# Kernel tuning notes

Hardware: AMD Instinct MI355X
Metric: run time of the kernel (lower is better)

The kernel has to match this reference:

```python
import jax, jax.numpy as jnp
import numpy as np

NUM_HEADS = 16
D_MODEL = 1024
D_K = D_MODEL // NUM_HEADS


def setup_inputs() -> dict:
    key = jax.random.key(0)
    ks = jax.random.split(key, 11)
    B, S, D = 4, 2048, D_MODEL
    s = 1.0 / np.sqrt(D)
    return {
        "query": jax.random.normal(ks[0], (B, S, D), jnp.float32),
        "key": jax.random.normal(ks[1], (B, S, D), jnp.float32),
        "value": jax.random.normal(ks[2], (B, S, D), jnp.float32),
        "Wq": jax.random.normal(ks[3], (D, D), jnp.float32) * s,
        "bq": jnp.zeros((D,), jnp.float32),
        "Wk": jax.random.normal(ks[4], (D, D), jnp.float32) * s,
        "bk": jnp.zeros((D,), jnp.float32),
        "Wv": jax.random.normal(ks[5], (D, D), jnp.float32) * s,
        "bv": jnp.zeros((D,), jnp.float32),
        "Wo": jax.random.normal(ks[6], (D, D), jnp.float32) * s,
        "bo": jnp.zeros((D,), jnp.float32),
    }


def reference(query, key, value, Wq, bq, Wk, bk, Wv, bv, Wo, bo):
    B, S, D = query.shape
    H, dk = NUM_HEADS, D_K
    # linear projections (torch Linear: x @ W.T + b)
    q = query @ Wq.T + bq
    k = key @ Wk.T + bk
    v = value @ Wv.T + bv
    # [B, S, D] -> [B, H, S, dk]
    q = q.reshape(B, S, H, dk).transpose(0, 2, 1, 3)
    k = k.reshape(B, S, H, dk).transpose(0, 2, 1, 3)
    v = v.reshape(B, S, H, dk).transpose(0, 2, 1, 3)
    # scaled dot-product attention (explicit scores, no mask, dropout unused in fwd)
    scores = jnp.einsum("bhqd,bhkd->bhqk", q, k) / jnp.sqrt(jnp.float32(dk))
    attn = jax.nn.softmax(scores, axis=-1)
    out = jnp.einsum("bhqk,bhkd->bhqd", attn, v)
    out = out.transpose(0, 2, 1, 3).reshape(B, S, D)
    return out @ Wo.T + bo
```

## Files before the change

kernel.cpp:

```cpp
#include <hip/hip_runtime.h>
#include <cstdint>
#include <cstddef>

typedef __bf16 bf16_t;
typedef __bf16 bf16x8 __attribute__((ext_vector_type(8)));
typedef __bf16 bf16x4 __attribute__((ext_vector_type(4)));
typedef float f32x4 __attribute__((ext_vector_type(4)));

static constexpr int SEQ = 2048;
static constexpr int DMODEL = 1024;
static constexpr int HEADS = 16;
static constexpr int DK = 64;
static constexpr int MROWS = 4 * SEQ;
static constexpr size_t NEC = (size_t)MROWS * DMODEL;
static constexpr size_t WEC = (size_t)DMODEL * DMODEL;

__global__ __launch_bounds__(256) void cast_w(const float* __restrict__ wq,
                                              const float* __restrict__ wk,
                                              const float* __restrict__ wv,
                                              const float* __restrict__ wo,
                                              bf16_t* __restrict__ out) {
  size_t i = (size_t)blockIdx.x * 256 + threadIdx.x;
  size_t e = i * 8;
  const float* src;
  size_t off;
  if (e < WEC) { src = wq; off = e; }
  else if (e < 2 * WEC) { src = wk; off = e - WEC; }
  else if (e < 3 * WEC) { src = wv; off = e - 2 * WEC; }
  else { src = wo; off = e - 3 * WEC; }
  const float4* p = reinterpret_cast<const float4*>(src + off);
  float4 a = p[0], b = p[1];
  bf16x8 o;
  o[0] = (bf16_t)a.x; o[1] = (bf16_t)a.y; o[2] = (bf16_t)a.z; o[3] = (bf16_t)a.w;
  o[4] = (bf16_t)b.x; o[5] = (bf16_t)b.y; o[6] = (bf16_t)b.z; o[7] = (bf16_t)b.w;
  *(reinterpret_cast<bf16x8*>(out + e)) = o;
}

__device__ __forceinline__ void async16(const bf16_t* g, bf16_t* l) {
  __builtin_amdgcn_global_load_lds((const __attribute__((address_space(1))) void*)g,
                                   (__attribute__((address_space(3))) void*)l,
                                   16, 0, 0);
}

__device__ __forceinline__ int lds_off(int m, int l4) {
  int lr = m >> 1;
  return lr * 64 + (((((m & 1) << 2) | l4) ^ (lr & 7)) << 3);
}

__global__ __launch_bounds__(512, 4) void gemm_qkv(const float* __restrict__ Aq,
                                                   const float* __restrict__ Ak,
                                                   const float* __restrict__ Av,
                                                   const bf16_t* __restrict__ Wbase,
                                                   const float* __restrict__ bq,
                                                   const float* __restrict__ bk,
                                                   const float* __restrict__ bv,
                                                   float scaleQ,
                                                   bf16_t* __restrict__ QKbase,
                                                   bf16_t* __restrict__ Vt) {
  __shared__ __align__(16) bf16_t smem[24576];
  bf16_t* sAb = smem;
  bf16_t* sBb = smem + 8192;
  const int tid = threadIdx.x;
  const int lane = tid & 63;
  const int w = tid >> 6;
  const int wm = w >> 2, wn = w & 3;
  const int l16 = lane & 15, l4 = lane >> 4;

  int bid = blockIdx.x;
  int swz = (bid & 7) * 96 + (bid >> 3);
  const int seg = swz >> 8;
  const int inner = swz & 255;
  const float* Afp = seg == 0 ? Aq : (seg == 1 ? Ak : Av);
  const bf16_t* Bw = Wbase + (size_t)seg * WEC;
  const float* bias = seg == 0 ? bq : (seg == 1 ? bk : bv);
  const float scale = seg == 0 ? scaleQ : 1.0f;
  const int bm = inner >> 2, bn = inner & 3;
  const int m0 = bm << 7, n0 = bn << 8;

  const int sg = (lane & 7) ^ ((lane >> 3) & 7);
  const int mS = 2 * (w * 8 + (lane >> 3)) + (sg >> 2);
  const int gS = (sg & 3) * 8;

  f32x4 acc[4][4] = {};
  float4 ra0, ra1;

  auto loadA = [&](int k0) {
    const float* p = Afp + (size_t)(m0 + mS) * DMODEL + k0 + gS;
    ra0 = *reinterpret_cast<const float4*>(p);
    ra1 = *reinterpret_cast<const float4*>(p + 4);
  };
  auto writeA = [&](int bb) {
    bf16x8 o;
    o[0] = (bf16_t)ra0.x; o[1] = (bf16_t)ra0.y; o[2] = (bf16_t)ra0.z; o[3] = (bf16_t)ra0.w;
    o[4] = (bf16_t)ra1.x; o[5] = (bf16_t)ra1.y; o[6] = (bf16_t)ra1.z; o[7] = (bf16_t)ra1.w;
    *reinterpret_cast<bf16x8*>(&sAb[bb * 4096 + w * 512 + lane * 8]) = o;
  };
  auto stageB = [&](int bb, int k0) {
    async16(Bw + (size_t)(n0 + mS) * DMODEL + k0 + gS, &sBb[bb * 8192 + w * 512]);
    async16(Bw + (size_t)(n0 + 128 + mS) * DMODEL + k0 + gS, &sBb[bb * 8192 + 4096 + w * 512]);
  };

  loadA(0);
  stageB(0, 0);
  writeA(0);
  __syncthreads();
  const int NKT = DMODEL / 32;
  for (int t = 0; t < NKT; ++t) {
    if (t + 1 < NKT) {
      loadA((t + 1) * 32);
      stageB((t + 1) & 1, (t + 1) * 32);
    }
    const bf16_t* bA = &sAb[(t & 1) * 4096];
    const bf16_t* bB = &sBb[(t & 1) * 8192];
    bf16x8 af[4], bf[4];
#pragma unroll
    for (int f = 0; f < 4; ++f)
      af[f] = *reinterpret_cast<const bf16x8*>(&bA[lds_off(wm * 64 + f * 16 + l16, l4)]);
#pragma unroll
    for (int j = 0; j < 4; ++j)
      bf[j] = *reinterpret_cast<const bf16x8*>(&bB[lds_off(wn * 64 + j * 16 + l16, l4)]);
    __builtin_amdgcn_s_setprio(1);
#pragma unroll
    for (int i = 0; i < 4; ++i)
#pragma unroll
      for (int j = 0; j < 4; ++j)
        acc[i][j] = __builtin_amdgcn_mfma_f32_16x16x32_bf16(af[i], bf[j], acc[i][j], 0, 0, 0);
    __builtin_amdgcn_s_setprio(0);
    if (t + 1 < NKT) writeA((t + 1) & 1);
    __syncthreads();
  }

  float bj[4];
#pragma unroll
  for (int j = 0; j < 4; ++j) bj[j] = bias[n0 + wn * 64 + j * 16 + l16];

  const int hglob = bn * 4 + wn;
  bf16_t* patch = smem + w * 3072;

  if (seg < 2) {
    bf16_t* outQK = QKbase + (size_t)seg * NEC;
#pragma unroll
    for (int h2 = 0; h2 < 2; ++h2) {
#pragma unroll
      for (int ii = 0; ii < 2; ++ii) {
        int i = h2 * 2 + ii;
#pragma unroll
        for (int j = 0; j < 4; ++j) {
#pragma unroll
          for (int r = 0; r < 4; ++r) {
            float v = (acc[i][j][r] + bj[j]) * scale;
            patch[(ii * 16 + l4 * 4 + r) * 72 + j * 16 + l16] = (bf16_t)v;
          }
        }
      }
#pragma unroll
      for (int kk = 0; kk < 4; ++kk) {
        int row = kk * 8 + (lane >> 3);
        int doff = (lane & 7) * 8;
        bf16x8 ch = *reinterpret_cast<const bf16x8*>(&patch[row * 72 + doff]);
        int m = m0 + wm * 64 + h2 * 32 + row;
        int b = m >> 11, s = m & 2047;
        *reinterpret_cast<bf16x8*>(
            &outQK[(((size_t)(b * HEADS + hglob) * SEQ + s) << 6) + doff]) = ch;
      }
    }
  } else {
#pragma unroll
    for (int h2 = 0; h2 < 2; ++h2) {
#pragma unroll
      for (int ii = 0; ii < 2; ++ii) {
        int i = h2 * 2 + ii;
#pragma unroll
        for (int j = 0; j < 4; ++j) {
          bf16x4 pk;
#pragma unroll
          for (int r = 0; r < 4; ++r) pk[r] = (bf16_t)(acc[i][j][r] + bj[j]);
          *reinterpret_cast<bf16x4*>(
              &patch[(j * 16 + l16) * 48 + ii * 16 + l4 * 4]) = pk;
        }
      }
#pragma unroll
      for (int kk = 0; kk < 4; ++kk) {
        int d = kk * 16 + (lane >> 2);
        int soff = (lane & 3) * 8;
        bf16x8 ch = *reinterpret_cast<const bf16x8*>(&patch[d * 48 + soff]);
        int m = m0 + wm * 64 + h2 * 32;
        int b = m >> 11, s = (m & 2047) + soff;
        *reinterpret_cast<bf16x8*>(
            &Vt[((size_t)(b * HEADS + hglob) * DK + d) * SEQ + s]) = ch;
      }
    }
  }
}

__global__ __launch_bounds__(256, 4) void gemm_out(const bf16_t* __restrict__ A,
                                                   const bf16_t* __restrict__ Bw,
                                                   const float* __restrict__ bias,
                                                   float* __restrict__ Cout) {
  __shared__ __align__(16) bf16_t sA[2][128 * 32];
  __shared__ __align__(16) bf16_t sB[2][128 * 32];
  const int tid = threadIdx.x;
  const int lane = tid & 63;
  const int wv = tid >> 6;
  const int l16 = lane & 15, l4 = lane >> 4;

  int bid = blockIdx.x;
  int swz = (bid & 7) * 64 + (bid >> 3);
  const int bm = swz >> 3, bn = swz & 7;
  const int m0 = bm << 7, n0 = bn << 7;
  const int wr = (wv >> 1) * 64, wc = (wv & 1) * 64;

  const int sg = (lane & 7) ^ ((lane >> 3) & 7);
  const int mS = 2 * (wv * 8 + (lane >> 3)) + (sg >> 2);
  const int gS = (sg & 3) * 8;

  f32x4 acc[4][4] = {};

  auto stage = [&](int bb, int k0) {
#pragma unroll
    for (int c = 0; c < 2; ++c) {
      async16(A + (size_t)(m0 + c * 64 + mS) * DMODEL + k0 + gS, &sA[bb][c * 2048 + wv * 512]);
      async16(Bw + (size_t)(n0 + c * 64 + mS) * DMODEL + k0 + gS, &sB[bb][c * 2048 + wv * 512]);
    }
  };

  stage(0, 0);
  __syncthreads();
  const int NKT = DMODEL / 32;
  for (int t = 0; t < NKT; ++t) {
    if (t + 1 < NKT) stage((t + 1) & 1, (t + 1) * 32);
    const bf16_t* bA = sA[t & 1];
    const bf16_t* bB = sB[t & 1];
    bf16x8 afrag[4], bfrag[4];
#pragma unroll
    for (int f = 0; f < 4; ++f) {
      afrag[f] = *reinterpret_cast<const bf16x8*>(&bA[lds_off(wr + f * 16 + l16, l4)]);
      bfrag[f] = *reinterpret_cast<const bf16x8*>(&bB[lds_off(wc + f * 16 + l16, l4)]);
    }
    __builtin_amdgcn_s_setprio(1);
#pragma unroll
    for (int i = 0; i < 4; ++i)
#pragma unroll
      for (int j = 0; j < 4; ++j)
        acc[i][j] = __builtin_amdgcn_mfma_f32_16x16x32_bf16(afrag[i], bfrag[j], acc[i][j], 0, 0, 0);
    __builtin_amdgcn_s_setprio(0);
    __syncthreads();
  }

  float bj[4];
#pragma unroll
  for (int j = 0; j < 4; ++j) bj[j] = bias[n0 + wc + j * 16 + l16];

#pragma unroll
  for (int i = 0; i < 4; ++i) {
#pragma unroll
    for (int j = 0; j < 4; ++j) {
#pragma unroll
      for (int r = 0; r < 4; ++r) {
        int m = m0 + wr + i * 16 + l4 * 4 + r;
        int n = n0 + wc + j * 16 + l16;
        Cout[(size_t)m * DMODEL + n] = acc[i][j][r] + bj[j];
      }
    }
  }
}

__device__ __forceinline__ int kvsrc_row(int r) {
  return (r & 32) | (((r >> 3) & 1) << 4) | (((r >> 2) & 1) << 3) |
         (((r >> 4) & 1) << 2) | (r & 3);
}

__global__ __launch_bounds__(512, 2) void attn_kernel(const bf16_t* __restrict__ Q,
                                                      const bf16_t* __restrict__ Kp,
                                                      const bf16_t* __restrict__ Vt,
                                                      bf16_t* __restrict__ AO) {
  __shared__ __align__(16) bf16_t sK[2][64 * 64];
  __shared__ __align__(16) bf16_t sV[2][64 * 64];
  const int tid = threadIdx.x;
  const int lane = tid & 63;
  const int wv = tid >> 6;
  const int l16 = lane & 15, l4 = lane >> 4;
  const int sub8 = lane >> 3, c8 = lane & 7;

  const int nq = SEQ / 256;
  int bid = blockIdx.x;
  int swz = (bid & 7) * 64 + (bid >> 3);
  const int bh = swz / nq, qt = swz % nq;
  const int b = bh >> 4, h = bh & 15;
  const bf16_t* Qh = Q + (size_t)bh * SEQ * DK;
  const bf16_t* Kh = Kp + (size_t)bh * SEQ * DK;
  const bf16_t* Vh = Vt + (size_t)bh * DK * SEQ;
  const int q0 = qt * 256 + wv * 32;

  bf16x8 aq[2][2];
#pragma unroll
  for (int s = 0; s < 2; ++s)
#pragma unroll
    for (int hf = 0; hf < 2; ++hf)
      aq[s][hf] = *reinterpret_cast<const bf16x8*>(
          &Qh[(size_t)(q0 + s * 16 + l16) * DK + hf * 32 + l4 * 8]);

  bf16x8 ones;
#pragma unroll
  for (int i = 0; i < 8; ++i) ones[i] = (bf16_t)1.0f;

  f32x4 o[2][4] = {};
  f32x4 lacc[2] = {};

  auto stage = [&](int buf, int kv0) {
    int r = wv * 8 + sub8;
    int kvr = kvsrc_row(r);
    int cs = (c8 ^ sub8) << 3;
    async16(Kh + (size_t)(kv0 + kvr) * DK + cs, &sK[buf][wv * 512]);
    async16(Vh + (size_t)r * SEQ + kv0 + cs, &sV[buf][wv * 512]);
  };

  auto compute = [&](int buf) {
    const bf16_t* bK = sK[buf];
    const bf16_t* bV = sV[buf];
    f32x4 sc[2][4] = {};
    __builtin_amdgcn_s_setprio(1);
#pragma unroll
    for (int t = 0; t < 4; ++t) {
      bf16x8 kf0 = *reinterpret_cast<const bf16x8*>(
          &bK[(t * 16 + l16) * 64 + ((l4 ^ (l16 & 7)) << 3)]);
      bf16x8 kf1 = *reinterpret_cast<const bf16x8*>(
          &bK[(t * 16 + l16) * 64 + (((4 + l4) ^ (l16 & 7)) << 3)]);
#pragma unroll
      for (int s = 0; s < 2; ++s) {
        sc[s][t] = __builtin_amdgcn_mfma_f32_16x16x32_bf16(kf0, aq[s][0], sc[s][t], 0, 0, 0);
        sc[s][t] = __builtin_amdgcn_mfma_f32_16x16x32_bf16(kf1, aq[s][1], sc[s][t], 0, 0, 0);
      }
    }
    __builtin_amdgcn_s_setprio(0);
    bf16x8 pa[2][2];
#pragma unroll
    for (int s = 0; s < 2; ++s) {
#pragma unroll
      for (int t = 0; t < 4; ++t) {
#pragma unroll
        for (int j = 0; j < 4; ++j) {
          pa[s][t >> 1][(t & 1) * 4 + j] = (bf16_t)__builtin_amdgcn_exp2f(sc[s][t][j]);
        }
      }
    }
    __builtin_amdgcn_s_setprio(1);
#pragma unroll
    for (int nb = 0; nb < 4; ++nb) {
      bf16x8 vf0 = *reinterpret_cast<const bf16x8*>(
          &bV[(nb * 16 + l16) * 64 + ((l4 ^ (l16 & 7)) << 3)]);
      bf16x8 vf1 = *reinterpret_cast<const bf16x8*>(
          &bV[(nb * 16 + l16) * 64 + (((4 + l4) ^ (l16 & 7)) << 3)]);
#pragma unroll
      for (int s = 0; s < 2; ++s) {
        o[s][nb] = __builtin_amdgcn_mfma_f32_16x16x32_bf16(pa[s][0], vf0, o[s][nb], 0, 0, 0);
        o[s][nb] = __builtin_amdgcn_mfma_f32_16x16x32_bf16(pa[s][1], vf1, o[s][nb], 0, 0, 0);
      }
    }
#pragma unroll
    for (int s = 0; s < 2; ++s) {
      lacc[s] = __builtin_amdgcn_mfma_f32_16x16x32_bf16(pa[s][0], ones, lacc[s], 0, 0, 0);
      lacc[s] = __builtin_amdgcn_mfma_f32_16x16x32_bf16(pa[s][1], ones, lacc[s], 0, 0, 0);
    }
    __builtin_amdgcn_s_setprio(0);
  };

  stage(0, 0);
  __syncthreads();
  const int NT = SEQ / 64;
  for (int it = 0; it < NT; ++it) {
    if (it + 1 < NT) stage((it + 1) & 1, (it + 1) * 64);
    compute(it & 1);
    __syncthreads();
  }

#pragma unroll
  for (int s = 0; s < 2; ++s) {
#pragma unroll
    for (int j = 0; j < 4; ++j) {
      float inv = 1.0f / lacc[s][j];
      int qrow = q0 + s * 16 + l4 * 4 + j;
#pragma unroll
      for (int nb = 0; nb < 4; ++nb)
        AO[((size_t)(b * SEQ + qrow)) * DMODEL + h * DK + nb * 16 + l16] =
            (bf16_t)(o[s][nb][j] * inv);
    }
  }
}

extern "C" void kernel_launch(void* const* d_in, const int* in_sizes, int n_in,
                              void* d_out, int out_size, void* d_ws, size_t ws_size,
                              hipStream_t stream) {
  const float* query = (const float*)d_in[0];
  const float* key_i = (const float*)d_in[1];
  const float* value = (const float*)d_in[2];
  const float* Wq = (const float*)d_in[3];
  const float* bq = (const float*)d_in[4];
  const float* Wk = (const float*)d_in[5];
  const float* bk = (const float*)d_in[6];
  const float* Wv = (const float*)d_in[7];
  const float* bv = (const float*)d_in[8];
  const float* Wo = (const float*)d_in[9];
  const float* bo = (const float*)d_in[10];
  float* out = (float*)d_out;

  bf16_t* wqb = (bf16_t*)d_ws;
  bf16_t* wob = wqb + 3 * WEC;
  bf16_t* Qp = wob + WEC;
  bf16_t* Kp = Qp + NEC;
  bf16_t* Vt = Kp + NEC;
  bf16_t* AO = Vt + NEC;

  cast_w<<<dim3((unsigned)(4 * WEC / 8 / 256)), dim3(256), 0, stream>>>(
      Wq, Wk, Wv, Wo, wqb);

  const float cexp = 0.18033688f;
  gemm_qkv<<<dim3(768), dim3(512), 0, stream>>>(query, key_i, value, wqb,
                                                bq, bk, bv, cexp, Qp, Vt);

  attn_kernel<<<dim3(4 * HEADS * (SEQ / 256)), 512, 0, stream>>>(Qp, Kp, Vt, AO);

  gemm_out<<<dim3(512), dim3(256), 0, stream>>>(AO, wob, bo, out);
}
```

Before: 168.3 us.

## Deepen A prefetch in QKV GEMM; load out-proj A fragments directly to registers

In the QKV projection GEMM, the K loop is unrolled by two with two register sets for the fp32 A tile. Each A tile is now loaded two iterations ahead rather than one, which gives more time to hide global-load latency. In the output projection GEMM, the A operand no longer goes through shared memory: each wave loads its MFMA fragments straight from global into registers, double-buffered, and only B is staged in LDS. This cuts LDS traffic and footprint, but it adds register pressure under launch_bounds(256,4) and relies on less coalesced global reads of A.

```diff
diff --git a/kernel.cpp b/kernel.cpp
--- a/kernel.cpp
+++ b/kernel.cpp
@@ -82,36 +82,26 @@
   const int gS = (sg & 3) * 8;
 
   f32x4 acc[4][4] = {};
-  float4 ra0, ra1;
-
-  auto loadA = [&](int k0) {
+  float4 rA0, rA1, rB0, rB1;
+
+  auto loadA = [&](float4& r0, float4& r1, int k0) {
     const float* p = Afp + (size_t)(m0 + mS) * DMODEL + k0 + gS;
-    ra0 = *reinterpret_cast<const float4*>(p);
-    ra1 = *reinterpret_cast<const float4*>(p + 4);
-  };
-  auto writeA = [&](int bb) {
+    r0 = *reinterpret_cast<const float4*>(p);
+    r1 = *reinterpret_cast<const float4*>(p + 4);
+  };
+  auto writeA = [&](int bb, const float4& r0, const float4& r1) {
     bf16x8 o;
-    o[0] = (bf16_t)ra0.x; o[1] = (bf16_t)ra0.y; o[2] = (bf16_t)ra0.z; o[3] = (bf16_t)ra0.w;
-    o[4] = (bf16_t)ra1.x; o[5] = (bf16_t)ra1.y; o[6] = (bf16_t)ra1.z; o[7] = (bf16_t)ra1.w;
+    o[0] = (bf16_t)r0.x; o[1] = (bf16_t)r0.y; o[2] = (bf16_t)r0.z; o[3] = (bf16_t)r0.w;
+    o[4] = (bf16_t)r1.x; o[5] = (bf16_t)r1.y; o[6] = (bf16_t)r1.z; o[7] = (bf16_t)r1.w;
     *reinterpret_cast<bf16x8*>(&sAb[bb * 4096 + w * 512 + lane * 8]) = o;
   };
   auto stageB = [&](int bb, int k0) {
     async16(Bw + (size_t)(n0 + mS) * DMODEL + k0 + gS, &sBb[bb * 8192 + w * 512]);
     async16(Bw + (size_t)(n0 + 128 + mS) * DMODEL + k0 + gS, &sBb[bb * 8192 + 4096 + w * 512]);
   };
-
-  loadA(0);
-  stageB(0, 0);
-  writeA(0);
-  __syncthreads();
-  const int NKT = DMODEL / 32;
-  for (int t = 0; t < NKT; ++t) {
-    if (t + 1 < NKT) {
-      loadA((t + 1) * 32);
-      stageB((t + 1) & 1, (t + 1) * 32);
-    }
-    const bf16_t* bA = &sAb[(t & 1) * 4096];
-    const bf16_t* bB = &sBb[(t & 1) * 8192];
+  auto computeT = [&](int bb) {
+    const bf16_t* bA = &sAb[bb * 4096];
+    const bf16_t* bB = &sBb[bb * 8192];
     bf16x8 af[4], bf[4];
 #pragma unroll
     for (int f = 0; f < 4; ++f)
@@ -126,7 +116,24 @@
       for (int j = 0; j < 4; ++j)
         acc[i][j] = __builtin_amdgcn_mfma_f32_16x16x32_bf16(af[i], bf[j], acc[i][j], 0, 0, 0);
     __builtin_amdgcn_s_setprio(0);
-    if (t + 1 < NKT) writeA((t + 1) & 1);
+  };
+
+  const int NKT = DMODEL / 32;
+  loadA(rA0, rA1, 0);
+  stageB(0, 0);
+  writeA(0, rA0, rA1);
+  loadA(rB0, rB1, 32);
+  __syncthreads();
+  for (int t = 0; t < NKT; t += 2) {
+    if (t + 2 < NKT) loadA(rA0, rA1, (t + 2) * 32);
+    if (t + 1 < NKT) stageB(1, (t + 1) * 32);
+    computeT(0);
+    if (t + 1 < NKT) writeA(1, rB0, rB1);
+    __syncthreads();
+    if (t + 3 < NKT) loadA(rB0, rB1, (t + 3) * 32);
+    if (t + 2 < NKT) stageB(0, (t + 2) * 32);
+    computeT(1);
+    if (t + 2 < NKT) writeA(0, rA0, rA1);
     __syncthreads();
   }
 
@@ -197,7 +204,6 @@
                                                    const bf16_t* __restrict__ Bw,
                                                    const float* __restrict__ bias,
                                                    float* __restrict__ Cout) {
-  __shared__ __align__(16) bf16_t sA[2][128 * 32];
   __shared__ __align__(16) bf16_t sB[2][128 * 32];
   const int tid = threadIdx.x;
   const int lane = tid & 63;
@@ -215,35 +221,49 @@
   const int gS = (sg & 3) * 8;
 
   f32x4 acc[4][4] = {};
-
-  auto stage = [&](int bb, int k0) {
-#pragma unroll
-    for (int c = 0; c < 2; ++c) {
-      async16(A + (size_t)(m0 + c * 64 + mS) * DMODEL + k0 + gS, &sA[bb][c * 2048 + wv * 512]);
+  bf16x8 afE[4], afO[4];
+
+  auto loadAf = [&](bf16x8* af, int k0) {
+#pragma unroll
+    for (int f = 0; f < 4; ++f)
+      af[f] = *reinterpret_cast<const bf16x8*>(
+          &A[(size_t)(m0 + wr + f * 16 + l16) * DMODEL + k0 + l4 * 8]);
+  };
+  auto stageB = [&](int bb, int k0) {
+#pragma unroll
+    for (int c = 0; c < 2; ++c)
       async16(Bw + (size_t)(n0 + c * 64 + mS) * DMODEL + k0 + gS, &sB[bb][c * 2048 + wv * 512]);
-    }
-  };
-
-  stage(0, 0);
+  };
+  auto computeT = [&](const bf16x8* af, int bb) {
+    bf16x8 bf[4];
+#pragma unroll
+    for (int j = 0; j < 4; ++j)
+      bf[j] = *reinterpret_cast<const bf16x8*>(&sB[bb][lds_off(wc + j * 16 + l16, l4)]);
+    __builtin_amdgcn_s_setprio(1);
+#pragma unroll
+    for (int i = 0; i < 4; ++i)
+#pragma unroll
+      for (int j = 0; j < 4; ++j)
+        acc[i][j] = __builtin_amdgcn_mfma_f32_16x16x32_bf16(af[i], bf[j], acc[i][j], 0, 0, 0);
+    __builtin_amdgcn_s_setprio(0);
+  };
+
+  const int NKT = DMODEL / 32;
+  loadAf(afE, 0);
+  stageB(0, 0);
   __syncthreads();
-  const int NKT = DMODEL / 32;
-  for (int t = 0; t < NKT; ++t) {
-    if (t + 1 < NKT) stage((t + 1) & 1, (t + 1) * 32);
-    const bf16_t* bA = sA[t & 1];
-    const bf16_t* bB = sB[t & 1];
-    bf16x8 afrag[4], bfrag[4];
-#pragma unroll
-    for (int f = 0; f < 4; ++f) {
-      afrag[f] = *reinterpret_cast<const bf16x8*>(&bA[lds_off(wr + f * 16 + l16, l4)]);
-      bfrag[f] = *reinterpret_cast<const bf16x8*>(&bB[lds_off(wc + f * 16 + l16, l4)]);
-    }
-    __builtin_amdgcn_s_setprio(1);
-#pragma unroll
-    for (int i = 0; i < 4; ++i)
-#pragma unroll
-      for (int j = 0; j < 4; ++j)
-        acc[i][j] = __builtin_amdgcn_mfma_f32_16x16x32_bf16(afrag[i], bfrag[j], acc[i][j], 0, 0, 0);
-    __builtin_amdgcn_s_setprio(0);
+  for (int t = 0; t < NKT; t += 2) {
+    if (t + 1 < NKT) {
+      loadAf(afO, (t + 1) * 32);
+      stageB(1, (t + 1) * 32);
+    }
+    computeT(afE, 0);
+    __syncthreads();
+    if (t + 2 < NKT) {
+      loadAf(afE, (t + 2) * 32);
+      stageB(0, (t + 2) * 32);
+    }
+    computeT(afO, 1);
     __syncthreads();
   }
 
```

Measured after the change: 212.9 us. +26.5%, slower.

## Stage fp32 A tiles asynchronously into LDS and convert to bf16 on fragment load

Applied to the files above, without the earlier changes.

The QKV projection GEMM now loads the fp32 activation tile straight into LDS with global_load_lds, where before it went through registers, was cast to bf16 and written to LDS. The bf16 conversion moves to the point where fragments are read from LDS, using an XOR swizzle on the fp32 layout. The weight tile goes from a double buffer to a single buffer, with an extra barrier placed after the B fragments are read and before the next B is staged. The intent is to free registers and overlap A loads asynchronously. The cost is double the LDS traffic for A, conversions repeated in the inner loop, and an extra barrier per k-step.

```diff
diff --git a/kernel.cpp b/kernel.cpp
--- a/kernel.cpp
+++ b/kernel.cpp
@@ -36,7 +36,7 @@
   *(reinterpret_cast<bf16x8*>(out + e)) = o;
 }
 
-__device__ __forceinline__ void async16(const bf16_t* g, bf16_t* l) {
+__device__ __forceinline__ void async16(const void* g, void* l) {
   __builtin_amdgcn_global_load_lds((const __attribute__((address_space(1))) void*)g,
                                    (__attribute__((address_space(3))) void*)l,
                                    16, 0, 0);
@@ -58,13 +58,14 @@
                                                    bf16_t* __restrict__ QKbase,
                                                    bf16_t* __restrict__ Vt) {
   __shared__ __align__(16) bf16_t smem[24576];
-  bf16_t* sAb = smem;
-  bf16_t* sBb = smem + 8192;
+  float* sAf = reinterpret_cast<float*>(smem);
+  bf16_t* sBb = smem + 16384;
   const int tid = threadIdx.x;
   const int lane = tid & 63;
   const int w = tid >> 6;
   const int wm = w >> 2, wn = w & 3;
   const int l16 = lane & 15, l4 = lane >> 4;
+  const int sub8 = lane >> 3, c8 = lane & 7;
 
   int bid = blockIdx.x;
   int swz = (bid & 7) * 96 + (bid >> 3);
@@ -77,48 +78,51 @@
   const int bm = inner >> 2, bn = inner & 3;
   const int m0 = bm << 7, n0 = bn << 8;
 
-  const int sg = (lane & 7) ^ ((lane >> 3) & 7);
-  const int mS = 2 * (w * 8 + (lane >> 3)) + (sg >> 2);
+  const int sg = c8 ^ sub8;
+  const int mS = 2 * (w * 8 + sub8) + (sg >> 2);
   const int gS = (sg & 3) * 8;
+  const int rA = w * 8 + sub8;
+  const int gA = (c8 ^ sub8) * 4;
 
   f32x4 acc[4][4] = {};
-  float4 ra0, ra1;
-
-  auto loadA = [&](int k0) {
-    const float* p = Afp + (size_t)(m0 + mS) * DMODEL + k0 + gS;
-    ra0 = *reinterpret_cast<const float4*>(p);
-    ra1 = *reinterpret_cast<const float4*>(p + 4);
+
+  auto stageA = [&](int bb, int k0) {
+#pragma unroll
+    for (int c = 0; c < 2; ++c)
+      async16(Afp + (size_t)(m0 + c * 64 + rA) * DMODEL + k0 + gA,
+              sAf + bb * 4096 + c * 2048 + w * 256);
   };
-  auto writeA = [&](int bb) {
-    bf16x8 o;
-    o[0] = (bf16_t)ra0.x; o[1] = (bf16_t)ra0.y; o[2] = (bf16_t)ra0.z; o[3] = (bf16_t)ra0.w;
-    o[4] = (bf16_t)ra1.x; o[5] = (bf16_t)ra1.y; o[6] = (bf16_t)ra1.z; o[7] = (bf16_t)ra1.w;
-    *reinterpret_cast<bf16x8*>(&sAb[bb * 4096 + w * 512 + lane * 8]) = o;
+  auto stageB = [&](int k0) {
+    async16(Bw + (size_t)(n0 + mS) * DMODEL + k0 + gS, sBb + w * 512);
+    async16(Bw + (size_t)(n0 + 128 + mS) * DMODEL + k0 + gS, sBb + 4096 + w * 512);
   };
-  auto stageB = [&](int bb, int k0) {
-    async16(Bw + (size_t)(n0 + mS) * DMODEL + k0 + gS, &sBb[bb * 8192 + w * 512]);
-    async16(Bw + (size_t)(n0 + 128 + mS) * DMODEL + k0 + gS, &sBb[bb * 8192 + 4096 + w * 512]);
-  };
-
-  loadA(0);
-  stageB(0, 0);
-  writeA(0);
+
+  stageA(0, 0);
+  stageB(0);
   __syncthreads();
   const int NKT = DMODEL / 32;
   for (int t = 0; t < NKT; ++t) {
+    bf16x8 bf[4];
+#pragma unroll
+    for (int j = 0; j < 4; ++j)
+      bf[j] = *reinterpret_cast<const bf16x8*>(&sBb[lds_off(wn * 64 + j * 16 + l16, l4)]);
+    __syncthreads();
     if (t + 1 < NKT) {
-      loadA((t + 1) * 32);
-      stageB((t + 1) & 1, (t + 1) * 32);
-    }
-    const bf16_t* bA = &sAb[(t & 1) * 4096];
-    const bf16_t* bB = &sBb[(t & 1) * 8192];
-    bf16x8 af[4], bf[4];
-#pragma unroll
-    for (int f = 0; f < 4; ++f)
-      af[f] = *reinterpret_cast<const bf16x8*>(&bA[lds_off(wm * 64 + f * 16 + l16, l4)]);
-#pragma unroll
-    for (int j = 0; j < 4; ++j)
-      bf[j] = *reinterpret_cast<const bf16x8*>(&bB[lds_off(wn * 64 + j * 16 + l16, l4)]);
+      stageA((t + 1) & 1, (t + 1) * 32);
+      stageB((t + 1) * 32);
+    }
+    const float* bA = sAf + (t & 1) * 4096;
+    bf16x8 af[4];
+#pragma unroll
+    for (int f = 0; f < 4; ++f) {
+      int R = wm * 64 + f * 16 + l16;
+      int s0 = (2 * l4) ^ (R & 7);
+      const float* rb = bA + R * 32;
+      f32x4 a0 = *reinterpret_cast<const f32x4*>(rb + s0 * 4);
+      f32x4 a1 = *reinterpret_cast<const f32x4*>(rb + (s0 ^ 1) * 4);
+#pragma unroll
+      for (int e = 0; e < 4; ++e) { af[f][e] = (bf16_t)a0[e]; af[f][4 + e] = (bf16_t)a1[e]; }
+    }
     __builtin_amdgcn_s_setprio(1);
 #pragma unroll
     for (int i = 0; i < 4; ++i)
@@ -126,7 +130,6 @@
       for (int j = 0; j < 4; ++j)
         acc[i][j] = __builtin_amdgcn_mfma_f32_16x16x32_bf16(af[i], bf[j], acc[i][j], 0, 0, 0);
     __builtin_amdgcn_s_setprio(0);
-    if (t + 1 < NKT) writeA((t + 1) & 1);
     __syncthreads();
   }
 
@@ -155,8 +158,8 @@
       }
 #pragma unroll
       for (int kk = 0; kk < 4; ++kk) {
-        int row = kk * 8 + (lane >> 3);
-        int doff = (lane & 7) * 8;
+        int row = kk * 8 + sub8;
+        int doff = c8 * 8;
         bf16x8 ch = *reinterpret_cast<const bf16x8*>(&patch[row * 72 + doff]);
         int m = m0 + wm * 64 + h2 * 32 + row;
         int b = m >> 11, s = m & 2047;
```

After: 166.8 us (median of 3 runs). About the same (-0.9%).
